# Kernel tuning notes

Hardware: AMD Instinct MI355X
Metric: run time of the kernel (lower is better)

Reference implementation:

```python
import jax, jax.numpy as jnp
import numpy as np

H, B, F, D1, D21, D22, C = 10, 16384, 4, 2048, 2048, 2048, 2
OBS_X, OBS_Y, RADIUS = 40.0, 15.0, 6.0


def setup_inputs() -> dict:
    key = jax.random.key(0)
    ks = jax.random.split(key, 12)
    s = 0.02  # weight scale
    return {
        'x':   jax.random.normal(ks[0], (B, F), jnp.float32),
        'W1':  jax.random.normal(ks[1], (H, F, D1), jnp.float32) * s,
        'b1':  jnp.zeros((H, D1), jnp.float32),
        'W21': jax.random.normal(ks[2], (H, D1, D21), jnp.float32) * s,
        'b21': jnp.zeros((H, D21), jnp.float32),
        'W22': jax.random.normal(ks[3], (H, D1, D22), jnp.float32) * s,
        'b22': jnp.zeros((H, D22), jnp.float32),
        'W31': jax.random.normal(ks[4], (H, D21, C), jnp.float32) * s,
        'b31': jnp.zeros((H, C), jnp.float32),
        'W32': jax.random.normal(ks[5], (H, D22, C), jnp.float32) * s,
        'b32': jnp.zeros((H, C), jnp.float32),
        'wt':  jnp.ones((H,), jnp.float32),
        'mean': jax.random.normal(ks[6], (F,), jnp.float32),
        'std':  jnp.ones((F,), jnp.float32),
        'sgn': 1,
        'itr': 0,
    }


def reference(x, W1, b1, W21, b21, W22, b22, W31, b31, W32, b32, wt, mean, std, sgn, itr):
    # x: [B,F]; un-normalized state x0 = x*std + mean
    x0 = x * std + mean

    # --- 10-head small-MLP ensemble (batched over heads via einsum) ---
    h1  = jax.nn.relu(jnp.einsum('bf,hfd->hbd', x, W1) + b1[:, None, :])      # [H,B,D1]
    x21 = jax.nn.relu(jnp.einsum('hbd,hde->hbe', h1, W21) + b21[:, None, :])  # [H,B,D21]
    x22 = jax.nn.relu(jnp.einsum('hbd,hde->hbe', h1, W22) + b22[:, None, :])  # [H,B,D22]
    x31 = jnp.einsum('hbe,hec->hbc', x21, W31) + b31[:, None, :]              # [H,B,C] nominal control
    x32 = 4.0 * jax.nn.sigmoid(jnp.einsum('hbe,hec->hbc', x22, W32) + b32[:, None, :])  # [H,B,C] CBF params

    # --- dCBF constraint (shared across heads; depends only on x0) ---
    px, py, theta, v = x0[:, 0], x0[:, 1], x0[:, 2], x0[:, 3]
    dx, dy = px - OBS_X, py - OBS_Y
    st, ct = jnp.sin(theta), jnp.cos(theta)
    barrier = dx * dx + dy * dy - RADIUS * RADIUS                 # [B]
    barrier_dot = 2.0 * dx * v * ct + 2.0 * dy * v * st          # [B]
    Lf2b = 2.0 * v * v                                            # [B]
    LgLfbu1 = -2.0 * dx * v * st + 2.0 * dy * v * ct
    LgLfbu2 = 2.0 * dx * ct + 2.0 * dy * st
    G = jnp.stack([-LgLfbu1, -LgLfbu2], axis=-1)                  # [B,C]

    # sgn == 1 -> same branch for every head (i==0 or sgn==1)
    h_rhs = Lf2b + (x32[..., 0] + x32[..., 1]) * barrier_dot + x32[..., 0] * x32[..., 1] * barrier  # [H,B]

    # --- batched QP: min 0.5 u'u - x31'u  s.t. G u <= h  (Q = I) ---
    # closed-form single-constraint active set: u = x31 - relu(G.x31 - h)/||G||^2 * G
    Gu = jnp.einsum('bc,hbc->hb', G, x31)                         # [H,B]
    GG = jnp.sum(G * G, axis=-1)                                  # [B]
    lam = jax.nn.relu(Gu - h_rhs) / GG                            # [H,B]
    u = x31 - lam[..., None] * G[None, :, :]                      # [H,B,C]

    # --- softmax-weighted ensemble sum ---
    w = jax.nn.softmax(wt)                                        # [H]
    return jnp.einsum('h,hbc->bc', w, u)                          # [B,C]
```

## Files before the change

kernel.cpp:

```cpp
#include <hip/hip_runtime.h>
#include <hip/hip_bf16.h>
#include <stdint.h>

#define H_  10
#define B_  16384
#define F_  4
#define D_  2048
#define C_  2

typedef __attribute__((ext_vector_type(8))) short  short8;
typedef __attribute__((ext_vector_type(4))) float  floatx4;
typedef __attribute__((ext_vector_type(2))) float  float2v;

typedef const uint32_t __attribute__((address_space(1))) gu32;
typedef uint32_t       __attribute__((address_space(3))) lu32;

__device__ __forceinline__ void async16(const void* g, void* l) {
    __builtin_amdgcn_global_load_lds((gu32*)g, (lu32*)l, 16, 0, 0);
}

__device__ __forceinline__ uint32_t packbf(float a, float b) {
    a = fmaxf(a, 0.f); b = fmaxf(b, 0.f);
    const uint32_t ax = __builtin_bit_cast(uint32_t, a) + 0x8000u;
    const uint32_t bx = __builtin_bit_cast(uint32_t, b) + 0x8000u;
    return (ax >> 16) | (bx & 0xFFFF0000u);
}

__device__ __forceinline__ uint32_t f2bf(float f) {
    union { float f; uint32_t u; } a; a.f = f;
    uint32_t u = a.u;
    u += 0x7FFF + ((u >> 16) & 1);
    return u >> 16;
}
__device__ __forceinline__ uint32_t pack2bf(float a, float b) {
    return f2bf(a) | (f2bf(b) << 16);
}


__global__ __launch_bounds__(256) void k_convert(
    const float* __restrict__ W21, const float* __restrict__ W22,
    uint16_t* __restrict__ W21t, uint16_t* __restrict__ W22t)
{
    __shared__ float tile[64][65];
    const int z = blockIdx.z;
    const int h = z % H_;
    const float* src = (z < H_ ? W21 : W22) + (size_t)h * D_ * D_;
    uint16_t*   dst  = (z < H_ ? W21t : W22t) + (size_t)h * D_ * D_;
    const int k0 = blockIdx.x * 64, n0 = blockIdx.y * 64;
    const int t = threadIdx.x;

    const int c4 = (t & 15) * 4;
    const int rb = (t >> 4) * 4;
#pragma unroll
    for (int i = 0; i < 4; i++) {
        const float4 v = *(const float4*)(src + (size_t)(k0 + rb + i) * D_ + n0 + c4);
        tile[rb + i][c4 + 0] = v.x; tile[rb + i][c4 + 1] = v.y;
        tile[rb + i][c4 + 2] = v.z; tile[rb + i][c4 + 3] = v.w;
    }
    __syncthreads();
    const int n = t >> 2;
    const int cb = (t & 3) * 2;
#pragma unroll
    for (int j = 0; j < 2; j++) {
        const int kk = (cb + j) * 8;
        uint32_t pk[4];
#pragma unroll
        for (int e = 0; e < 4; e++)
            pk[e] = pack2bf(tile[kk + 2 * e][n], tile[kk + 2 * e + 1][n]);
        *(uint4*)(dst + (size_t)(n0 + n) * D_ + k0 + kk) = make_uint4(pk[0], pk[1], pk[2], pk[3]);
    }
}

__global__ __launch_bounds__(256) void k_zero(uint4* p, int n4) {
    const int i = blockIdx.x * 256 + threadIdx.x;
    if (i < n4) p[i] = make_uint4(0u, 0u, 0u, 0u);
}

__global__ __launch_bounds__(256, 2) void k_gemm(
    const float* __restrict__ x, const float* __restrict__ W1, const float* __restrict__ b1,
    const uint16_t* __restrict__ W21t, const uint16_t* __restrict__ W22t,
    const float* __restrict__ b21, const float* __restrict__ b22,
    const float* __restrict__ W31, const float* __restrict__ W32,
    float* __restrict__ acc31, float* __restrict__ acc32)
{
    __shared__ uint4 At[1024];
    __shared__ uint4 Bt0[1024];
    __shared__ uint4 Bt1[1024];

    const int h = blockIdx.z;
    const int mBase = blockIdx.x * 128;
    const int nBase = blockIdx.y * 128;
    const int t = threadIdx.x;
    const int lane = t & 63, wid = t >> 6;
    const int q = lane >> 4, c15 = lane & 15;
    const int wm = wid >> 1, wn = wid & 1;

    const int k0 = (t & 7) * 8;
    const int mg = (t >> 3) * 4;

    float xv[4][4];
#pragma unroll
    for (int i = 0; i < 4; i++) {
        const float4 v = *(const float4*)(x + (size_t)(mBase + mg + i) * F_);
        xv[i][0] = v.x; xv[i][1] = v.y; xv[i][2] = v.z; xv[i][3] = v.w;
    }

    const int nb = wid * 32 + (lane >> 3);
    const int chunk = (lane & 7) ^ ((lane >> 3) & 7);
    const uint16_t* bsrc0 = W21t + (size_t)h * D_ * D_ + (size_t)(nBase + nb) * D_ + chunk * 8;
    const uint16_t* bsrc1 = W22t + (size_t)h * D_ * D_ + (size_t)(nBase + nb) * D_ + chunk * 8;

    const float* W1h = W1 + (size_t)h * F_ * D_;
    const float* b1h = b1 + (size_t)h * D_;

    floatx4 acc0[4][4], acc1[4][4];
    const floatx4 z4 = {0.f, 0.f, 0.f, 0.f};
#pragma unroll
    for (int mi = 0; mi < 4; mi++)
#pragma unroll
        for (int ni = 0; ni < 4; ni++) { acc0[mi][ni] = z4; acc1[mi][ni] = z4; }

    for (int kt = 0; kt < D_; kt += 64) {
        float2v w1v[4][4], b1v[4];
        {
            const float4 bb0 = *(const float4*)(b1h + kt + k0);
            const float4 bb1 = *(const float4*)(b1h + kt + k0 + 4);
            b1v[0] = (float2v){bb0.x, bb0.y}; b1v[1] = (float2v){bb0.z, bb0.w};
            b1v[2] = (float2v){bb1.x, bb1.y}; b1v[3] = (float2v){bb1.z, bb1.w};
#pragma unroll
            for (int f = 0; f < 4; f++) {
                const float4 a0 = *(const float4*)(W1h + f * D_ + kt + k0);
                const float4 a1 = *(const float4*)(W1h + f * D_ + kt + k0 + 4);
                w1v[f][0] = (float2v){a0.x, a0.y}; w1v[f][1] = (float2v){a0.z, a0.w};
                w1v[f][2] = (float2v){a1.x, a1.y}; w1v[f][3] = (float2v){a1.z, a1.w};
            }
        }
#pragma unroll
        for (int i = 0; i < 4; i++) {
            async16(bsrc0 + kt + i * (8 * D_), (char*)Bt0 + wid * 4096 + i * 1024);
            async16(bsrc1 + kt + i * (8 * D_), (char*)Bt1 + wid * 4096 + i * 1024);
        }
#pragma unroll
        for (int i = 0; i < 4; i++) {
            const int m = mg + i;
            float2v hv[4];
#pragma unroll
            for (int j = 0; j < 4; j++) hv[j] = b1v[j];
#pragma unroll
            for (int f = 0; f < 4; f++) {
                const float2v xs = {xv[i][f], xv[i][f]};
#pragma unroll
                for (int j = 0; j < 4; j++)
                    hv[j] = __builtin_elementwise_fma(xs, w1v[f][j], hv[j]);
            }
            At[m * 8 + ((t & 7) ^ (m & 7))] =
                make_uint4(packbf(hv[0].x, hv[0].y), packbf(hv[1].x, hv[1].y),
                           packbf(hv[2].x, hv[2].y), packbf(hv[3].x, hv[3].y));
        }
        __syncthreads();
#pragma unroll
        for (int s = 0; s < 2; s++) {
            short8 af[4];
#pragma unroll
            for (int mi = 0; mi < 4; mi++) {
                const int m = wm * 64 + mi * 16 + c15;
                af[mi] = __builtin_bit_cast(short8, At[m * 8 + ((s * 4 + q) ^ (c15 & 7))]);
            }
#pragma unroll
            for (int ni = 0; ni < 4; ni++) {
                const int n = wn * 64 + ni * 16 + c15;
                const int bidx = n * 8 + ((s * 4 + q) ^ (c15 & 7));
                const short8 bf0 = __builtin_bit_cast(short8, Bt0[bidx]);
#pragma unroll
                for (int mi = 0; mi < 4; mi++)
                    acc0[mi][ni] = __builtin_amdgcn_mfma_f32_16x16x32_bf16(af[mi], bf0, acc0[mi][ni], 0, 0, 0);
                const short8 bf1 = __builtin_bit_cast(short8, Bt1[bidx]);
#pragma unroll
                for (int mi = 0; mi < 4; mi++)
                    acc1[mi][ni] = __builtin_amdgcn_mfma_f32_16x16x32_bf16(af[mi], bf1, acc1[mi][ni], 0, 0, 0);
            }
        }
        __syncthreads();
    }

#pragma unroll
    for (int p = 0; p < 2; p++) {
        const float* b2p = (p == 0 ? b21 : b22) + (size_t)h * D_;
        const float* W3p = (p == 0 ? W31 : W32) + (size_t)h * D_ * C_;
        float* ab = (p == 0 ? acc31 : acc32) + (size_t)h * B_ * C_;
        float w3x[4], w3y[4], bs[4];
#pragma unroll
        for (int ni = 0; ni < 4; ni++) {
            const int n = nBase + wn * 64 + ni * 16 + c15;
            bs[ni] = b2p[n];
            const float2 w2 = *(const float2*)(W3p + n * 2);
            w3x[ni] = w2.x; w3y[ni] = w2.y;
        }
        float s0[16], s1[16];
#pragma unroll
        for (int mi = 0; mi < 4; mi++)
#pragma unroll
            for (int r = 0; r < 4; r++) {
                float t0 = 0.f, t1 = 0.f;
#pragma unroll
                for (int ni = 0; ni < 4; ni++) {
                    float v = (p == 0 ? acc0[mi][ni][r] : acc1[mi][ni][r]) + bs[ni];
                    v = fmaxf(v, 0.f);
                    t0 = fmaf(v, w3x[ni], t0);
                    t1 = fmaf(v, w3y[ni], t1);
                }
                s0[mi * 4 + r] = t0; s1[mi * 4 + r] = t1;
            }
#pragma unroll
        for (int off = 1; off < 16; off <<= 1)
#pragma unroll
            for (int i = 0; i < 16; i++) {
                s0[i] += __shfl_xor(s0[i], off, 64);
                s1[i] += __shfl_xor(s1[i], off, 64);
            }
        if (c15 == 0) {
#pragma unroll
            for (int mi = 0; mi < 4; mi++)
#pragma unroll
                for (int r = 0; r < 4; r++) {
                    const int row = mBase + wm * 64 + mi * 16 + q * 4 + r;
                    atomicAdd(&ab[row * C_ + 0], s0[mi * 4 + r]);
                    atomicAdd(&ab[row * C_ + 1], s1[mi * 4 + r]);
                }
        }
    }
}

__global__ __launch_bounds__(256) void k_final(
    const float* __restrict__ x,
    const float* __restrict__ acc31, const float* __restrict__ acc32,
    const float* __restrict__ b31, const float* __restrict__ b32,
    const float* __restrict__ wt, const float* __restrict__ mean,
    const float* __restrict__ stdv, float* __restrict__ out)
{
    const int b = blockIdx.x * 256 + threadIdx.x;
    const float4 xb = *(const float4*)(x + (size_t)b * 4);
    const float px = xb.x * stdv[0] + mean[0];
    const float py = xb.y * stdv[1] + mean[1];
    const float th = xb.z * stdv[2] + mean[2];
    const float v  = xb.w * stdv[3] + mean[3];
    const float dx = px - 40.0f, dy = py - 15.0f;
    const float st = sinf(th), ct = cosf(th);
    const float barrier = dx * dx + dy * dy - 36.0f;
    const float bdot = 2.f * dx * v * ct + 2.f * dy * v * st;
    const float Lf2b = 2.f * v * v;
    const float G0 = -(-2.f * dx * v * st + 2.f * dy * v * ct);
    const float G1 = -(2.f * dx * ct + 2.f * dy * st);
    const float GG = G0 * G0 + G1 * G1;

    float we[H_];
    float wmax = wt[0];
    for (int h = 1; h < H_; h++) wmax = fmaxf(wmax, wt[h]);
    float wsum = 0.f;
    for (int h = 0; h < H_; h++) { we[h] = expf(wt[h] - wmax); wsum += we[h]; }

    float o0 = 0.f, o1 = 0.f;
#pragma unroll
    for (int h = 0; h < H_; h++) {
        const size_t idx = ((size_t)h * B_ + b) * 2;
        const float x310 = acc31[idx]     + b31[h * 2];
        const float x311 = acc31[idx + 1] + b31[h * 2 + 1];
        const float z0 = acc32[idx]     + b32[h * 2];
        const float z1 = acc32[idx + 1] + b32[h * 2 + 1];
        const float x320 = 4.f / (1.f + expf(-z0));
        const float x321 = 4.f / (1.f + expf(-z1));
        const float hr = Lf2b + (x320 + x321) * bdot + x320 * x321 * barrier;
        const float Gu = G0 * x310 + G1 * x311;
        const float lam = fmaxf(Gu - hr, 0.f) / GG;
        o0 += we[h] * (x310 - lam * G0);
        o1 += we[h] * (x311 - lam * G1);
    }
    out[b * 2]     = o0 / wsum;
    out[b * 2 + 1] = o1 / wsum;
}

extern "C" void kernel_launch(void* const* d_in, const int* in_sizes, int n_in,
                              void* d_out, int out_size, void* d_ws, size_t ws_size,
                              hipStream_t stream)
{
    const float* x    = (const float*)d_in[0];
    const float* W1   = (const float*)d_in[1];
    const float* b1   = (const float*)d_in[2];
    const float* W21  = (const float*)d_in[3];
    const float* b21  = (const float*)d_in[4];
    const float* W22  = (const float*)d_in[5];
    const float* b22  = (const float*)d_in[6];
    const float* W31  = (const float*)d_in[7];
    const float* b31  = (const float*)d_in[8];
    const float* W32  = (const float*)d_in[9];
    const float* b32  = (const float*)d_in[10];
    const float* wt   = (const float*)d_in[11];
    const float* mean = (const float*)d_in[12];
    const float* stdv = (const float*)d_in[13];
    float* out = (float*)d_out;

    char* ws = (char*)d_ws;
    uint16_t* W21t = (uint16_t*)(ws);
    uint16_t* W22t = (uint16_t*)(ws + 83886080);
    float* acc31   = (float*)(ws + 167772160);
    float* acc32   = (float*)(ws + 169082880);

    k_convert<<<dim3(32, 32, 20), 256, 0, stream>>>(W21, W22, W21t, W22t);
    k_zero<<<dim3(640), 256, 0, stream>>>((uint4*)acc31, 163840);
    k_gemm<<<dim3(128, 16, 10), 256, 0, stream>>>(x, W1, b1, W21t, W22t,
                                                  b21, b22, W31, W32, acc31, acc32);
    k_final<<<dim3(64), 256, 0, stream>>>(x, acc31, acc32, b31, b32, wt, mean, stdv, out);
}
```

Measured before the change: 3.587 ms.

## Precompute h1 per head and use 256x256 double-buffered GEMM tiles

Splits the layer-1 computation into a separate per-head kernel that writes h1 in bf16 to a workspace buffer. The main GEMM then streams both A and B from global memory into LDS through async loads. It uses 256x256 tiles with 512 threads, double buffering, a four-phase ping-pong schedule with barriers and setprio, and a grid remapping chosen for L2 locality. W21 and W22 are concatenated so one block covers either half of the N dimension. This trades the per-tile recomputation of h1 and the smaller tiles for extra h1 memory traffic and 20 more kernel launches.

```diff
diff --git a/kernel.cpp b/kernel.cpp
--- a/kernel.cpp
+++ b/kernel.cpp
@@ -10,7 +10,6 @@
 
 typedef __attribute__((ext_vector_type(8))) short  short8;
 typedef __attribute__((ext_vector_type(4))) float  floatx4;
-typedef __attribute__((ext_vector_type(2))) float  float2v;
 
 typedef const uint32_t __attribute__((address_space(1))) gu32;
 typedef uint32_t       __attribute__((address_space(3))) lu32;
@@ -18,6 +17,8 @@
 __device__ __forceinline__ void async16(const void* g, void* l) {
     __builtin_amdgcn_global_load_lds((gu32*)g, (lu32*)l, 16, 0, 0);
 }
+
+__device__ __forceinline__ short8 bc8(uint4 v) { return __builtin_bit_cast(short8, v); }
 
 __device__ __forceinline__ uint32_t packbf(float a, float b) {
     a = fmaxf(a, 0.f); b = fmaxf(b, 0.f);
@@ -39,13 +40,13 @@
 
 __global__ __launch_bounds__(256) void k_convert(
     const float* __restrict__ W21, const float* __restrict__ W22,
-    uint16_t* __restrict__ W21t, uint16_t* __restrict__ W22t)
+    uint16_t* __restrict__ Bc)
 {
     __shared__ float tile[64][65];
     const int z = blockIdx.z;
     const int h = z % H_;
     const float* src = (z < H_ ? W21 : W22) + (size_t)h * D_ * D_;
-    uint16_t*   dst  = (z < H_ ? W21t : W22t) + (size_t)h * D_ * D_;
+    uint16_t*   dst  = Bc + (size_t)h * 2 * D_ * D_ + (z < H_ ? 0 : (size_t)D_ * D_);
     const int k0 = blockIdx.x * 64, n0 = blockIdx.y * 64;
     const int t = threadIdx.x;
 
@@ -76,157 +77,248 @@
     if (i < n4) p[i] = make_uint4(0u, 0u, 0u, 0u);
 }
 
-__global__ __launch_bounds__(256, 2) void k_gemm(
-    const float* __restrict__ x, const float* __restrict__ W1, const float* __restrict__ b1,
-    const uint16_t* __restrict__ W21t, const uint16_t* __restrict__ W22t,
+__global__ __launch_bounds__(256) void k_h1(
+    const float* __restrict__ x, const float* __restrict__ W1,
+    const float* __restrict__ b1, uint16_t* __restrict__ h1t, int h)
+{
+    const int t = threadIdx.x;
+    const int kc = t & 127;
+    const int rh = t >> 7;
+    const int k0 = kc * 16;
+    const float* W1h = W1 + (size_t)h * F_ * D_;
+    float w[4][16], bb[16];
+#pragma unroll
+    for (int f = 0; f < 4; f++)
+#pragma unroll
+        for (int j = 0; j < 16; j += 4) {
+            const float4 v = *(const float4*)(W1h + f * D_ + k0 + j);
+            w[f][j] = v.x; w[f][j+1] = v.y; w[f][j+2] = v.z; w[f][j+3] = v.w;
+        }
+#pragma unroll
+    for (int j = 0; j < 16; j += 4) {
+        const float4 v = *(const float4*)(b1 + (size_t)h * D_ + k0 + j);
+        bb[j] = v.x; bb[j+1] = v.y; bb[j+2] = v.z; bb[j+3] = v.w;
+    }
+    const int rowBase = blockIdx.x * 16 + rh * 8;
+#pragma unroll
+    for (int rr = 0; rr < 8; rr++) {
+        const int row = rowBase + rr;
+        const float4 xv = *(const float4*)(x + (size_t)row * 4);
+        uint32_t pk[8];
+#pragma unroll
+        for (int j = 0; j < 16; j += 2) {
+            float aa = fmaf(xv.x, w[0][j], bb[j]);
+            aa = fmaf(xv.y, w[1][j], aa);
+            aa = fmaf(xv.z, w[2][j], aa);
+            aa = fmaf(xv.w, w[3][j], aa);
+            float bv = fmaf(xv.x, w[0][j+1], bb[j+1]);
+            bv = fmaf(xv.y, w[1][j+1], bv);
+            bv = fmaf(xv.z, w[2][j+1], bv);
+            bv = fmaf(xv.w, w[3][j+1], bv);
+            pk[j >> 1] = packbf(aa, bv);
+        }
+        uint16_t* d = h1t + (size_t)row * D_ + k0;
+        *(uint4*)d       = make_uint4(pk[0], pk[1], pk[2], pk[3]);
+        *(uint4*)(d + 8) = make_uint4(pk[4], pk[5], pk[6], pk[7]);
+    }
+}
+
+__global__ __launch_bounds__(512, 2) void k_gemm(
+    const uint16_t* __restrict__ h1t, const uint16_t* __restrict__ Bc,
     const float* __restrict__ b21, const float* __restrict__ b22,
     const float* __restrict__ W31, const float* __restrict__ W32,
-    float* __restrict__ acc31, float* __restrict__ acc32)
+    float* __restrict__ acc31, float* __restrict__ acc32, int h)
 {
-    __shared__ uint4 At[1024];
-    __shared__ uint4 Bt0[1024];
-    __shared__ uint4 Bt1[1024];
-
-    const int h = blockIdx.z;
-    const int mBase = blockIdx.x * 128;
-    const int nBase = blockIdx.y * 128;
+    extern __shared__ uint4 smem[];
+    uint4* Asl = smem;
+    uint4* Bsl = smem + 4096;
+
+    const int bid = blockIdx.x;
+    const int wg  = (bid & 7) * 128 + (bid >> 3);
+    const int mBase = (wg & 63) * 256;
+    const int nBase = (wg >> 6) * 256;
+
     const int t = threadIdx.x;
     const int lane = t & 63, wid = t >> 6;
-    const int q = lane >> 4, c15 = lane & 15;
-    const int wm = wid >> 1, wn = wid & 1;
-
-    const int k0 = (t & 7) * 8;
-    const int mg = (t >> 3) * 4;
-
-    float xv[4][4];
-#pragma unroll
-    for (int i = 0; i < 4; i++) {
-        const float4 v = *(const float4*)(x + (size_t)(mBase + mg + i) * F_);
-        xv[i][0] = v.x; xv[i][1] = v.y; xv[i][2] = v.z; xv[i][3] = v.w;
-    }
-
-    const int nb = wid * 32 + (lane >> 3);
-    const int chunk = (lane & 7) ^ ((lane >> 3) & 7);
-    const uint16_t* bsrc0 = W21t + (size_t)h * D_ * D_ + (size_t)(nBase + nb) * D_ + chunk * 8;
-    const uint16_t* bsrc1 = W22t + (size_t)h * D_ * D_ + (size_t)(nBase + nb) * D_ + chunk * 8;
-
-    const float* W1h = W1 + (size_t)h * F_ * D_;
-    const float* b1h = b1 + (size_t)h * D_;
-
-    floatx4 acc0[4][4], acc1[4][4];
+    const int c15 = lane & 15, q = lane >> 4;
+    const int wm = wid >> 2, wn = wid & 3;
+
+    const int srow   = lane >> 3;
+    const int schunk = (lane & 7) ^ srow;
+    const int sldA   = wid * 64;
+
+    const uint16_t* Ag = h1t + (size_t)(mBase + wid * 8 + srow) * D_ + schunk * 8;
+    const uint16_t* Bg = Bc + (size_t)h * (4096 * (size_t)D_)
+                            + (size_t)(nBase + wid * 8 + srow) * D_ + schunk * 8;
+
+    auto stageA = [&](int buf, int half, int kt) {
+#pragma unroll
+        for (int i = 0; i < 2; i++)
+            async16(Ag + (size_t)((half * 128 + i * 64) * D_ + kt),
+                    Asl + buf * 2048 + half * 1024 + i * 512 + sldA);
+    };
+    auto stageB = [&](int buf, int half, int kt) {
+#pragma unroll
+        for (int i = 0; i < 2; i++)
+            async16(Bg + (size_t)((half * 128 + i * 64) * D_ + kt),
+                    Bsl + buf * 2048 + half * 1024 + i * 512 + sldA);
+    };
+
+    const int axor  = c15 & 7;
+    const int ck0   = q ^ axor;
+    const int ck1   = (q + 4) ^ axor;
+    const int abase = (wm * 128 + c15) * 8;
+    const int bbase = (wn * 64 + c15) * 8;
+
+    floatx4 acc[8][4];
     const floatx4 z4 = {0.f, 0.f, 0.f, 0.f};
 #pragma unroll
-    for (int mi = 0; mi < 4; mi++)
-#pragma unroll
-        for (int ni = 0; ni < 4; ni++) { acc0[mi][ni] = z4; acc1[mi][ni] = z4; }
-
-    for (int kt = 0; kt < D_; kt += 64) {
-        float2v w1v[4][4], b1v[4];
-        {
-            const float4 bb0 = *(const float4*)(b1h + kt + k0);
-            const float4 bb1 = *(const float4*)(b1h + kt + k0 + 4);
-            b1v[0] = (float2v){bb0.x, bb0.y}; b1v[1] = (float2v){bb0.z, bb0.w};
-            b1v[2] = (float2v){bb1.x, bb1.y}; b1v[3] = (float2v){bb1.z, bb1.w};
-#pragma unroll
-            for (int f = 0; f < 4; f++) {
-                const float4 a0 = *(const float4*)(W1h + f * D_ + kt + k0);
-                const float4 a1 = *(const float4*)(W1h + f * D_ + kt + k0 + 4);
-                w1v[f][0] = (float2v){a0.x, a0.y}; w1v[f][1] = (float2v){a0.z, a0.w};
-                w1v[f][2] = (float2v){a1.x, a1.y}; w1v[f][3] = (float2v){a1.z, a1.w};
-            }
-        }
-#pragma unroll
-        for (int i = 0; i < 4; i++) {
-            async16(bsrc0 + kt + i * (8 * D_), (char*)Bt0 + wid * 4096 + i * 1024);
-            async16(bsrc1 + kt + i * (8 * D_), (char*)Bt1 + wid * 4096 + i * 1024);
-        }
-#pragma unroll
-        for (int i = 0; i < 4; i++) {
-            const int m = mg + i;
-            float2v hv[4];
-#pragma unroll
-            for (int j = 0; j < 4; j++) hv[j] = b1v[j];
-#pragma unroll
-            for (int f = 0; f < 4; f++) {
-                const float2v xs = {xv[i][f], xv[i][f]};
-#pragma unroll
-                for (int j = 0; j < 4; j++)
-                    hv[j] = __builtin_elementwise_fma(xs, w1v[f][j], hv[j]);
-            }
-            At[m * 8 + ((t & 7) ^ (m & 7))] =
-                make_uint4(packbf(hv[0].x, hv[0].y), packbf(hv[1].x, hv[1].y),
-                           packbf(hv[2].x, hv[2].y), packbf(hv[3].x, hv[3].y));
-        }
-        __syncthreads();
-#pragma unroll
-        for (int s = 0; s < 2; s++) {
-            short8 af[4];
-#pragma unroll
-            for (int mi = 0; mi < 4; mi++) {
-                const int m = wm * 64 + mi * 16 + c15;
-                af[mi] = __builtin_bit_cast(short8, At[m * 8 + ((s * 4 + q) ^ (c15 & 7))]);
-            }
+    for (int mi = 0; mi < 8; mi++)
+#pragma unroll
+        for (int ni = 0; ni < 4; ni++) acc[mi][ni] = z4;
+
+    stageA(0, 0, 0);  stageA(0, 1, 0);
+    stageB(0, 0, 0);  stageB(0, 1, 0);
+    stageA(1, 0, 64); stageA(1, 1, 64);
+    asm volatile("s_waitcnt vmcnt(4)" ::: "memory");
+    __builtin_amdgcn_sched_barrier(0);
+    __builtin_amdgcn_s_barrier();
+
+    int cur = 0;
+    for (int tt = 0; tt < 32; ++tt) {
+        const int ktB = (tt < 31 ? tt + 1 : 31) * 64;
+        const int ktA = (tt < 30 ? tt + 2 : 31) * 64;
+        const uint4* Ab = Asl + cur * 2048;
+        const uint4* Bb = Bsl + cur * 2048;
+        const int nxt = cur ^ 1;
+
+        short8 a0[4][2], a1[4][2], b0f[2][2], b1f[2][2];
+
+#pragma unroll
+        for (int mi = 0; mi < 4; mi++) {
+            a0[mi][0] = bc8(Ab[abase + mi * 128 + ck0]);
+            a0[mi][1] = bc8(Ab[abase + mi * 128 + ck1]);
+        }
+#pragma unroll
+        for (int ni = 0; ni < 2; ni++) {
+            b0f[ni][0] = bc8(Bb[bbase + ni * 128 + ck0]);
+            b0f[ni][1] = bc8(Bb[bbase + ni * 128 + ck1]);
+        }
+        __builtin_amdgcn_s_barrier();
+        asm volatile("s_waitcnt lgkmcnt(0)" ::: "memory");
+        __builtin_amdgcn_sched_barrier(0);
+        __builtin_amdgcn_s_setprio(1);
+#pragma unroll
+        for (int mi = 0; mi < 4; mi++)
+#pragma unroll
+            for (int ni = 0; ni < 2; ni++) {
+                acc[mi][ni] = __builtin_amdgcn_mfma_f32_16x16x32_bf16(a0[mi][0], b0f[ni][0], acc[mi][ni], 0, 0, 0);
+                acc[mi][ni] = __builtin_amdgcn_mfma_f32_16x16x32_bf16(a0[mi][1], b0f[ni][1], acc[mi][ni], 0, 0, 0);
+            }
+        __builtin_amdgcn_s_setprio(0);
+        __builtin_amdgcn_s_barrier();
+
+#pragma unroll
+        for (int ni = 0; ni < 2; ni++) {
+            b1f[ni][0] = bc8(Bb[bbase + (ni + 2) * 128 + ck0]);
+            b1f[ni][1] = bc8(Bb[bbase + (ni + 2) * 128 + ck1]);
+        }
+        stageB(nxt, 0, ktB);
+        __builtin_amdgcn_s_barrier();
+        asm volatile("s_waitcnt lgkmcnt(0)" ::: "memory");
+        __builtin_amdgcn_sched_barrier(0);
+        __builtin_amdgcn_s_setprio(1);
+#pragma unroll
+        for (int mi = 0; mi < 4; mi++)
+#pragma unroll
+            for (int ni = 0; ni < 2; ni++) {
+                acc[mi][ni + 2] = __builtin_amdgcn_mfma_f32_16x16x32_bf16(a0[mi][0], b1f[ni][0], acc[mi][ni + 2], 0, 0, 0);
+                acc[mi][ni + 2] = __builtin_amdgcn_mfma_f32_16x16x32_bf16(a0[mi][1], b1f[ni][1], acc[mi][ni + 2], 0, 0, 0);
+            }
+        __builtin_amdgcn_s_setprio(0);
+        __builtin_amdgcn_s_barrier();
+
+#pragma unroll
+        for (int mi = 0; mi < 4; mi++) {
+            a1[mi][0] = bc8(Ab[abase + (mi + 4) * 128 + ck0]);
+            a1[mi][1] = bc8(Ab[abase + (mi + 4) * 128 + ck1]);
+        }
+        stageB(nxt, 1, ktB);
+        __builtin_amdgcn_s_barrier();
+        asm volatile("s_waitcnt lgkmcnt(0)" ::: "memory");
+        __builtin_amdgcn_sched_barrier(0);
+        __builtin_amdgcn_s_setprio(1);
+#pragma unroll
+        for (int mi = 0; mi < 4; mi++)
+#pragma unroll
+            for (int ni = 0; ni < 2; ni++) {
+                acc[mi + 4][ni] = __builtin_amdgcn_mfma_f32_16x16x32_bf16(a1[mi][0], b0f[ni][0], acc[mi + 4][ni], 0, 0, 0);
+                acc[mi + 4][ni] = __builtin_amdgcn_mfma_f32_16x16x32_bf16(a1[mi][1], b0f[ni][1], acc[mi + 4][ni], 0, 0, 0);
+            }
+        __builtin_amdgcn_s_setprio(0);
+        __builtin_amdgcn_s_barrier();
+
+        stageA(cur, 0, ktA);
+        stageA(cur, 1, ktA);
+        asm volatile("s_waitcnt vmcnt(4)" ::: "memory");
+        __builtin_amdgcn_sched_barrier(0);
+        __builtin_amdgcn_s_barrier();
+        __builtin_amdgcn_s_setprio(1);
+#pragma unroll
+        for (int mi = 0; mi < 4; mi++)
+#pragma unroll
+            for (int ni = 0; ni < 2; ni++) {
+                acc[mi + 4][ni + 2] = __builtin_amdgcn_mfma_f32_16x16x32_bf16(a1[mi][0], b1f[ni][0], acc[mi + 4][ni + 2], 0, 0, 0);
+                acc[mi + 4][ni + 2] = __builtin_amdgcn_mfma_f32_16x16x32_bf16(a1[mi][1], b1f[ni][1], acc[mi + 4][ni + 2], 0, 0, 0);
+            }
+        __builtin_amdgcn_s_setprio(0);
+        __builtin_amdgcn_s_barrier();
+
+        cur = nxt;
+    }
+
+    const int p    = nBase >> 11;
+    const int nloc = nBase & 2047;
+    const float* b2p = (p ? b22 : b21) + (size_t)h * D_;
+    const float* W3p = (p ? W32 : W31) + (size_t)h * D_ * C_;
+    float* ab = (p ? acc32 : acc31) + (size_t)h * B_ * C_;
+
+    float w3x[4], w3y[4], bs[4];
+#pragma unroll
+    for (int ni = 0; ni < 4; ni++) {
+        const int e = nloc + wn * 64 + ni * 16 + c15;
+        bs[ni] = b2p[e];
+        const float2 w2 = *(const float2*)(W3p + e * 2);
+        w3x[ni] = w2.x; w3y[ni] = w2.y;
+    }
+#pragma unroll
+    for (int mi = 0; mi < 8; mi++) {
+        float s0[4], s1[4];
+#pragma unroll
+        for (int r = 0; r < 4; r++) {
+            float t0 = 0.f, t1 = 0.f;
 #pragma unroll
             for (int ni = 0; ni < 4; ni++) {
-                const int n = wn * 64 + ni * 16 + c15;
-                const int bidx = n * 8 + ((s * 4 + q) ^ (c15 & 7));
-                const short8 bf0 = __builtin_bit_cast(short8, Bt0[bidx]);
-#pragma unroll
-                for (int mi = 0; mi < 4; mi++)
-                    acc0[mi][ni] = __builtin_amdgcn_mfma_f32_16x16x32_bf16(af[mi], bf0, acc0[mi][ni], 0, 0, 0);
-                const short8 bf1 = __builtin_bit_cast(short8, Bt1[bidx]);
-#pragma unroll
-                for (int mi = 0; mi < 4; mi++)
-                    acc1[mi][ni] = __builtin_amdgcn_mfma_f32_16x16x32_bf16(af[mi], bf1, acc1[mi][ni], 0, 0, 0);
-            }
-        }
-        __syncthreads();
-    }
-
-#pragma unroll
-    for (int p = 0; p < 2; p++) {
-        const float* b2p = (p == 0 ? b21 : b22) + (size_t)h * D_;
-        const float* W3p = (p == 0 ? W31 : W32) + (size_t)h * D_ * C_;
-        float* ab = (p == 0 ? acc31 : acc32) + (size_t)h * B_ * C_;
-        float w3x[4], w3y[4], bs[4];
-#pragma unroll
-        for (int ni = 0; ni < 4; ni++) {
-            const int n = nBase + wn * 64 + ni * 16 + c15;
-            bs[ni] = b2p[n];
-            const float2 w2 = *(const float2*)(W3p + n * 2);
-            w3x[ni] = w2.x; w3y[ni] = w2.y;
-        }
-        float s0[16], s1[16];
-#pragma unroll
-        for (int mi = 0; mi < 4; mi++)
+                float v = fmaxf(acc[mi][ni][r] + bs[ni], 0.f);
+                t0 = fmaf(v, w3x[ni], t0);
+                t1 = fmaf(v, w3y[ni], t1);
+            }
+            s0[r] = t0; s1[r] = t1;
+        }
+#pragma unroll
+        for (int off = 1; off < 16; off <<= 1)
 #pragma unroll
             for (int r = 0; r < 4; r++) {
-                float t0 = 0.f, t1 = 0.f;
-#pragma unroll
-                for (int ni = 0; ni < 4; ni++) {
-                    float v = (p == 0 ? acc0[mi][ni][r] : acc1[mi][ni][r]) + bs[ni];
-                    v = fmaxf(v, 0.f);
-                    t0 = fmaf(v, w3x[ni], t0);
-                    t1 = fmaf(v, w3y[ni], t1);
-                }
-                s0[mi * 4 + r] = t0; s1[mi * 4 + r] = t1;
-            }
-#pragma unroll
-        for (int off = 1; off < 16; off <<= 1)
-#pragma unroll
-            for (int i = 0; i < 16; i++) {
-                s0[i] += __shfl_xor(s0[i], off, 64);
-                s1[i] += __shfl_xor(s1[i], off, 64);
+                s0[r] += __shfl_xor(s0[r], off, 64);
+                s1[r] += __shfl_xor(s1[r], off, 64);
             }
         if (c15 == 0) {
 #pragma unroll
-            for (int mi = 0; mi < 4; mi++)
-#pragma unroll
-                for (int r = 0; r < 4; r++) {
-                    const int row = mBase + wm * 64 + mi * 16 + q * 4 + r;
-                    atomicAdd(&ab[row * C_ + 0], s0[mi * 4 + r]);
-                    atomicAdd(&ab[row * C_ + 1], s1[mi * 4 + r]);
-                }
+            for (int r = 0; r < 4; r++) {
+                const int row = mBase + wm * 128 + mi * 16 + q * 4 + r;
+                atomicAdd(&ab[row * C_ + 0], s0[r]);
+                atomicAdd(&ab[row * C_ + 1], s1[r]);
+            }
         }
     }
 }
@@ -300,14 +392,24 @@
     float* out = (float*)d_out;
 
     char* ws = (char*)d_ws;
-    uint16_t* W21t = (uint16_t*)(ws);
-    uint16_t* W22t = (uint16_t*)(ws + 83886080);
+    uint16_t* Bc   = (uint16_t*)(ws);
     float* acc31   = (float*)(ws + 167772160);
     float* acc32   = (float*)(ws + 169082880);
-
-    k_convert<<<dim3(32, 32, 20), 256, 0, stream>>>(W21, W22, W21t, W22t);
+    uint16_t* h1t  = (uint16_t*)(ws + 170393600);
+
+    static bool attr_done = false;
+    if (!attr_done) {
+        hipFuncSetAttribute(reinterpret_cast<const void*>(k_gemm),
+                            hipFuncAttributeMaxDynamicSharedMemorySize, 131072);
+        attr_done = true;
+    }
+
+    k_convert<<<dim3(32, 32, 20), 256, 0, stream>>>(W21, W22, Bc);
     k_zero<<<dim3(640), 256, 0, stream>>>((uint4*)acc31, 163840);
-    k_gemm<<<dim3(128, 16, 10), 256, 0, stream>>>(x, W1, b1, W21t, W22t,
-                                                  b21, b22, W31, W32, acc31, acc32);
+    for (int h = 0; h < H_; ++h) {
+        k_h1<<<dim3(1024), 256, 0, stream>>>(x, W1, b1, h1t, h);
+        k_gemm<<<dim3(1024), 512, 131072, stream>>>(h1t, Bc, b21, b22, W31, W32,
+                                                    acc31, acc32, h);
+    }
     k_final<<<dim3(64), 256, 0, stream>>>(x, acc31, acc32, b31, b32, wt, mean, stdv, out);
 }
```

Result: slower. 3.828 ms (+6.7%).
